# Optimization experiments

Measured on AMD Instinct MI355X. Metric: run time of the kernel, lower is better.

The kernel has to match this reference:

```python
import jax, jax.numpy as jnp
import numpy as np

N, E, T = 10000, 50000, 80000   # nodes, edges, triplets
D, H, C, CF = 16, 128, 64, 64   # n_orb, hidden_dim, conv_dim, coeffs_dim


def l2norm(v):
    # matches torch F.normalize(dim=-1): x / max(||x||_2, 1e-12)
    return v / jnp.maximum(jnp.linalg.norm(v, axis=-1, keepdims=True), 1e-12)


def setup_inputs() -> dict:
    key = jax.random.key(0)
    ks = jax.random.split(key, 16)

    def w(k, i, o):
        return jax.random.normal(k, (i, o), jnp.float32) / np.sqrt(i).astype(np.float32)

    return {
        "x": jax.random.normal(ks[0], (N, H), jnp.float32),
        "cji": jax.random.normal(ks[1], (E, D, CF), jnp.float32),
        "robs": jax.random.normal(ks[2], (E, D), jnp.float32),
        "shbs": jax.random.normal(ks[3], (T, D), jnp.float32),
        "idx_i": jax.random.randint(ks[4], (E,), 0, N),
        "idx_j": jax.random.randint(ks[5], (E,), 0, N),
        "tri_idx_k": jax.random.randint(ks[6], (T,), 0, N),
        "edge_idx_kj": jax.random.randint(ks[7], (T,), 0, E),
        "edge_idx_ji": jax.random.randint(ks[8], (T,), 0, E),
        "W_nb": w(ks[9], H, 2 * C), "b_nb": jnp.zeros((2 * C,), jnp.float32),
        "W_c1": w(ks[10], CF, C),
        "W_c2": w(ks[11], C, 2 * C),
        "W_t3": w(ks[12], C, C), "b_t3": jnp.zeros((C,), jnp.float32),
        "W_n1": w(ks[13], 2 * C, C), "b_n1": jnp.zeros((C,), jnp.float32),
        "W_n2": w(ks[14], C, C), "b_n2": jnp.zeros((C,), jnp.float32),
        "W_na": w(ks[15], C, H),
    }


def reference(x, cji, robs, shbs, idx_i, idx_j, tri_idx_k, edge_idx_kj,
              edge_idx_ji, W_nb, b_nb, W_c1, W_c2, W_t3, b_t3, W_n1, b_n1,
              W_n2, b_n2, W_na):
    silu = jax.nn.silu
    # node_before_lin + chunk
    h = x @ W_nb + b_nb                       # [N, 2C]
    xq, xk = jnp.split(h, 2, axis=-1)         # each [N, C]
    # coeffs_before_lin: act -> Dense -> act -> Dense (no biases)
    c = silu(silu(cji) @ W_c1) @ W_c2         # [E, D, 2C]
    cji2, ckj = jnp.split(c, 2, axis=-1)      # each [E, D, C]
    # triplet gathers
    ckj_g = l2norm(ckj[edge_idx_kj])          # [T, D, C]
    tbo = l2norm(jnp.einsum('td,tdh->th', shbs * robs[edge_idx_kj], ckj_g))  # [T, C]
    tbw = tbo * jax.nn.sigmoid(xk[tri_idx_k])  # [T, C]
    # scatter triplets -> edges (dim_size = robs.size(0) = E)
    agg = jax.ops.segment_sum(tbw, edge_idx_ji, num_segments=E)  # [E, C]
    tbw2 = silu(agg) @ W_t3 + b_t3            # three_lin, [E, C]
    cji3 = l2norm(cji2 * (1.0 + tbw2[:, None, :]))  # cji + cji*w, normalized
    lcao = l2norm(jnp.einsum('ed,edh->eh', robs, cji3))  # [E, C]
    # node message: node_lin on concatenated endpoint features
    m = jnp.concatenate([xq[idx_i], xq[idx_j]], axis=-1)  # [E, 2C]
    m = silu(silu(m) @ W_n1 + b_n1) @ W_n2 + b_n2          # [E, C]
    out = x + jax.ops.segment_sum(lcao * m, idx_i, num_segments=N) @ W_na
    return out
```

## Files before the change

kernel.cpp:

```cpp
#include <hip/hip_runtime.h>
#include <hip/hip_bf16.h>

#define NN 10000
#define EE 50000
#define TT 80000
#define DD 16
#define HH 128
#define CC 64

typedef __hip_bfloat16 bf16;
typedef __attribute__((ext_vector_type(8))) short bf16x8;
typedef __attribute__((ext_vector_type(4))) short bf16x4;
typedef __attribute__((ext_vector_type(4))) float f32x4;

__device__ __forceinline__ float silu_f(float x) {
  return x * __builtin_amdgcn_rcpf(1.f + __expf(-x));
}
__device__ __forceinline__ float sigm_f(float x) {
  return __builtin_amdgcn_rcpf(1.f + __expf(-x));
}

__device__ __forceinline__ short f2bs(float x) {
  __hip_bfloat16 h = __float2bfloat16(x);
  short s;
  __builtin_memcpy(&s, &h, 2);
  return s;
}

__device__ __forceinline__ float rnorm_f(float ss) {
  return __builtin_amdgcn_rcpf(fmaxf(__builtin_amdgcn_sqrtf(ss), 1e-12f));
}

__device__ __forceinline__ void bf2x(unsigned u, float& lo, float& hi) {
  lo = __uint_as_float(u << 16);
  hi = __uint_as_float(u & 0xffff0000u);
}

#define ZERO_U4 960000

#define K2_BLOCKS 2048
#define K2_TILES 50000
__global__ __launch_bounds__(256, 2) void k_coeffs(
    const float* __restrict__ cji, const float* __restrict__ W_c1,
    const float* __restrict__ W_c2, bf16* __restrict__ cji2,
    bf16* __restrict__ ckjn, const float* __restrict__ x,
    const float* __restrict__ W_nb, const float* __restrict__ b_nb,
    float* __restrict__ sxq, float* __restrict__ sigxk,
    uint4* __restrict__ zero_p) {
  __shared__ __align__(16) float xs[16][HH];
  const int tid = threadIdx.x;
  const int bid = blockIdx.x;
  const int w = tid >> 6, l = tid & 63;
  const int lr = l & 15, lg = l >> 4;

  for (int i = bid * 256 + tid; i < ZERO_U4; i += K2_BLOCKS * 256)
    zero_p[i] = (uint4){0u, 0u, 0u, 0u};

  if (bid < NN / 16) {
    const int g = tid >> 7, c = tid & 127;
    const int nb = bid * 16 + g * 8;
#pragma unroll
    for (int i = 0; i < 8; ++i)
      xs[g * 8 + i][c] = x[(size_t)(nb + i) * HH + c];
    __syncthreads();
    float acc[8];
    const float bb = b_nb[c];
#pragma unroll
    for (int i = 0; i < 8; ++i) acc[i] = bb;
    for (int k = 0; k < HH; k += 4) {
      const float w0 = W_nb[(k + 0) * HH + c];
      const float w1 = W_nb[(k + 1) * HH + c];
      const float w2 = W_nb[(k + 2) * HH + c];
      const float w3 = W_nb[(k + 3) * HH + c];
#pragma unroll
      for (int i = 0; i < 8; ++i) {
        const float4 xv = *(const float4*)(&xs[g * 8 + i][k]);
        acc[i] = fmaf(xv.x, w0, acc[i]);
        acc[i] = fmaf(xv.y, w1, acc[i]);
        acc[i] = fmaf(xv.z, w2, acc[i]);
        acc[i] = fmaf(xv.w, w3, acc[i]);
      }
    }
    if (c < CC) {
#pragma unroll
      for (int i = 0; i < 8; ++i)
        sxq[(size_t)(nb + i) * CC + c] = silu_f(acc[i]);
    } else {
#pragma unroll
      for (int i = 0; i < 8; ++i)
        sigxk[(size_t)(nb + i) * CC + (c - CC)] = sigm_f(acc[i]);
    }
  }

  bf16x4 bw1[4][4];
  bf16x4 bw2[4][8];
#pragma unroll
  for (int rt = 0; rt < 4; ++rt)
#pragma unroll
    for (int kt = 0; kt < 4; ++kt) {
      bf16x4 t;
#pragma unroll
      for (int b = 0; b < 4; ++b)
        t[b] = f2bs(W_c1[(kt * 16 + lg * 4 + b) * 64 + rt * 16 + lr]);
      bw1[rt][kt] = t;
    }
#pragma unroll
  for (int kt = 0; kt < 4; ++kt)
#pragma unroll
    for (int ct = 0; ct < 8; ++ct) {
      bf16x4 t;
#pragma unroll
      for (int b = 0; b < 4; ++b)
        t[b] = f2bs(W_c2[(kt * 16 + lg * 4 + b) * 128 + ct * 16 + lr]);
      bw2[kt][ct] = t;
    }

  const int nwave = K2_BLOCKS * 4;
  int tile = bid * 4 + w;
  if (tile >= K2_TILES) return;

  float4 r[4];
#pragma unroll
  for (int kt = 0; kt < 4; ++kt)
    r[kt] = *(const float4*)(cji + (size_t)tile * 1024 + lr * 64 + kt * 16 + lg * 4);

  for (; tile < K2_TILES; tile += nwave) {
    bf16x4 sB[4];
#pragma unroll
    for (int kt = 0; kt < 4; ++kt) {
      bf16x4 t;
      t[0] = f2bs(silu_f(r[kt].x));
      t[1] = f2bs(silu_f(r[kt].y));
      t[2] = f2bs(silu_f(r[kt].z));
      t[3] = f2bs(silu_f(r[kt].w));
      sB[kt] = t;
    }

    const int next = tile + nwave;
    if (next < K2_TILES) {
#pragma unroll
      for (int kt = 0; kt < 4; ++kt)
        r[kt] = *(const float4*)(cji + (size_t)next * 1024 + lr * 64 + kt * 16 + lg * 4);
    }

    f32x4 acc1[4];
#pragma unroll
    for (int rt = 0; rt < 4; ++rt) acc1[rt] = (f32x4){0.f, 0.f, 0.f, 0.f};
    __builtin_amdgcn_s_setprio(1);
#pragma unroll
    for (int rt = 0; rt < 4; ++rt)
#pragma unroll
      for (int kt = 0; kt < 4; ++kt)
        acc1[rt] = __builtin_amdgcn_mfma_f32_16x16x16bf16_1k(bw1[rt][kt], sB[kt], acc1[rt], 0, 0, 0);
    __builtin_amdgcn_s_setprio(0);

    bf16x4 tf[4];
#pragma unroll
    for (int kt = 0; kt < 4; ++kt) {
      bf16x4 t;
#pragma unroll
      for (int b = 0; b < 4; ++b) t[b] = f2bs(silu_f(acc1[kt][b]));
      tf[kt] = t;
    }

    f32x4 acc2[8];
#pragma unroll
    for (int ct = 0; ct < 8; ++ct) acc2[ct] = (f32x4){0.f, 0.f, 0.f, 0.f};
    __builtin_amdgcn_s_setprio(1);
#pragma unroll
    for (int ct = 0; ct < 8; ++ct)
#pragma unroll
      for (int kt = 0; kt < 4; ++kt)
        acc2[ct] = __builtin_amdgcn_mfma_f32_16x16x16bf16_1k(tf[kt], bw2[kt][ct], acc2[ct], 0, 0, 0);
    __builtin_amdgcn_s_setprio(0);

    float rn[4];
#pragma unroll
    for (int j = 0; j < 4; ++j) {
      float ss = acc2[4][j] * acc2[4][j];
      ss = fmaf(acc2[5][j], acc2[5][j], ss);
      ss = fmaf(acc2[6][j], acc2[6][j], ss);
      ss = fmaf(acc2[7][j], acc2[7][j], ss);
#pragma unroll
      for (int m = 1; m < 16; m <<= 1) ss += __shfl_xor(ss, m, 64);
      rn[j] = rnorm_f(ss);
    }

    union { short h[16]; uint4 u[2]; } p;
#pragma unroll
    for (int ct = 0; ct < 4; ++ct)
#pragma unroll
      for (int j = 0; j < 4; ++j) p.h[ct * 4 + j] = f2bs(acc2[ct][j]);
    {
      uint4* d0 = (uint4*)(cji2 + (size_t)tile * 1024 + l * 16);
      d0[0] = p.u[0];
      d0[1] = p.u[1];
    }
#pragma unroll
    for (int ct = 0; ct < 4; ++ct)
#pragma unroll
      for (int j = 0; j < 4; ++j) p.h[ct * 4 + j] = f2bs(acc2[4 + ct][j] * rn[j]);
    {
      uint4* d1 = (uint4*)(ckjn + (size_t)tile * 1024 + l * 16);
      d1[0] = p.u[0];
      d1[1] = p.u[1];
    }
  }
}

#define K3_WAVES 20000
__global__ __launch_bounds__(256) void k_triplet(
    const bf16* __restrict__ ckjn, const float* __restrict__ shbs,
    const float* __restrict__ robs, const float* __restrict__ sigxk,
    const int* __restrict__ tri_idx_k, const int* __restrict__ edge_idx_kj,
    const int* __restrict__ edge_idx_ji, float* __restrict__ agg) {
  const int wid = (blockIdx.x * 256 + threadIdx.x) >> 6;
  const int l = threadIdx.x & 63;
  if (wid >= K3_WAVES) return;
  const int lq = l >> 4;
  const int t0 = wid * 4;

  int kj[4], kn[4], ji[4];
#pragma unroll
  for (int i = 0; i < 4; ++i) {
    kj[i] = edge_idx_kj[t0 + i];
    kn[i] = tri_idx_k[t0 + i];
    ji[i] = edge_idx_ji[t0 + i];
  }
  float4 sh[4], rb[4];
  uint4 u0[4], u1[4];
  float sx[4];
#pragma unroll
  for (int i = 0; i < 4; ++i) {
    sh[i] = *(const float4*)(shbs + (size_t)(t0 + i) * DD + lq * 4);
    rb[i] = *(const float4*)(robs + (size_t)kj[i] * DD + lq * 4);
    const uint4* b = (const uint4*)(ckjn + (size_t)kj[i] * 1024 + l * 16);
    u0[i] = b[0];
    u1[i] = b[1];
    sx[i] = sigxk[(size_t)kn[i] * CC + l];
  }

  float acc[4][4];
#pragma unroll
  for (int i = 0; i < 4; ++i) {
    const float w0 = sh[i].x * rb[i].x, w1 = sh[i].y * rb[i].y,
                w2 = sh[i].z * rb[i].z, w3 = sh[i].w * rb[i].w;
    float x0, x1, x2, x3;
    bf2x(u0[i].x, x0, x1); bf2x(u0[i].y, x2, x3);
    acc[i][0] = fmaf(w3, x3, fmaf(w2, x2, fmaf(w1, x1, w0 * x0)));
    bf2x(u0[i].z, x0, x1); bf2x(u0[i].w, x2, x3);
    acc[i][1] = fmaf(w3, x3, fmaf(w2, x2, fmaf(w1, x1, w0 * x0)));
    bf2x(u1[i].x, x0, x1); bf2x(u1[i].y, x2, x3);
    acc[i][2] = fmaf(w3, x3, fmaf(w2, x2, fmaf(w1, x1, w0 * x0)));
    bf2x(u1[i].z, x0, x1); bf2x(u1[i].w, x2, x3);
    acc[i][3] = fmaf(w3, x3, fmaf(w2, x2, fmaf(w1, x1, w0 * x0)));
  }
#pragma unroll
  for (int m = 16; m < 64; m <<= 1)
#pragma unroll
    for (int i = 0; i < 4; ++i)
#pragma unroll
      for (int q = 0; q < 4; ++q) acc[i][q] += __shfl_xor(acc[i][q], m, 64);

  float sel[4], ss[4];
#pragma unroll
  for (int i = 0; i < 4; ++i) {
    sel[i] = (lq == 0) ? acc[i][0] : (lq == 1) ? acc[i][1]
             : (lq == 2) ? acc[i][2] : acc[i][3];
    ss[i] = sel[i] * sel[i];
  }
#pragma unroll
  for (int m = 1; m < 64; m <<= 1)
#pragma unroll
    for (int i = 0; i < 4; ++i) ss[i] += __shfl_xor(ss[i], m, 64);
#pragma unroll
  for (int i = 0; i < 4; ++i) {
    const float tbw = sel[i] * rnorm_f(ss[i]) * sx[i];
    atomicAdd(&agg[(size_t)ji[i] * CC + l], tbw);
  }
}

#define K4A_TILES 3125
#define K4A_BLOCKS 256
__global__ __launch_bounds__(256, 2) void k_edge_a(
    const float* __restrict__ agg, const float* __restrict__ sxq,
    const int* __restrict__ idx_i, const int* __restrict__ idx_j,
    const float* __restrict__ W_t3, const float* __restrict__ b_t3,
    const float* __restrict__ W_n1, const float* __restrict__ b_n1,
    const float* __restrict__ W_n2, const float* __restrict__ b_n2,
    float* __restrict__ onew_buf, float* __restrict__ m_buf) {
  __shared__ __align__(16) float fbuf[4][16 * 68];
  __shared__ __align__(16) short sbuf[4][16 * 72];
  const int tid = threadIdx.x;
  const int w = tid >> 6, l = tid & 63;
  const int lr = l & 15, lg = l >> 4;
  float* fb = fbuf[w];
  short* sb = sbuf[w];

  bf16x8 bt3[2][4], bn1[4][4], bn2[2][4];
#pragma unroll
  for (int kt = 0; kt < 2; ++kt)
#pragma unroll
    for (int nt = 0; nt < 4; ++nt) {
      bf16x8 t;
#pragma unroll
      for (int b = 0; b < 8; ++b)
        t[b] = f2bs(W_t3[(kt * 32 + lg * 8 + b) * 64 + nt * 16 + lr]);
      bt3[kt][nt] = t;
    }
#pragma unroll
  for (int kt = 0; kt < 4; ++kt)
#pragma unroll
    for (int nt = 0; nt < 4; ++nt) {
      bf16x8 t;
#pragma unroll
      for (int b = 0; b < 8; ++b)
        t[b] = f2bs(W_n1[(kt * 32 + lg * 8 + b) * 64 + nt * 16 + lr]);
      bn1[kt][nt] = t;
    }
#pragma unroll
  for (int kt = 0; kt < 2; ++kt)
#pragma unroll
    for (int nt = 0; nt < 4; ++nt) {
      bf16x8 t;
#pragma unroll
      for (int b = 0; b < 8; ++b)
        t[b] = f2bs(W_n2[(kt * 32 + lg * 8 + b) * 64 + nt * 16 + lr]);
      bn2[kt][nt] = t;
    }
  float bt3c[4], bn1c[4], bn2c[4];
#pragma unroll
  for (int nt = 0; nt < 4; ++nt) {
    bt3c[nt] = b_t3[nt * 16 + lr];
    bn1c[nt] = b_n1[nt * 16 + lr];
    bn2c[nt] = b_n2[nt * 16 + lr];
  }

  for (int tile = blockIdx.x * 4 + w; tile < K4A_TILES; tile += K4A_BLOCKS * 4) {
    const int e = tile * 16 + lr;
    const int vi = idx_i[e], vj = idx_j[e];

    bf16x8 aagg[2];
#pragma unroll
    for (int kt = 0; kt < 2; ++kt) {
      const float4 u = *(const float4*)(agg + (size_t)e * 64 + kt * 32 + lg * 8);
      const float4 v = *(const float4*)(agg + (size_t)e * 64 + kt * 32 + lg * 8 + 4);
      bf16x8 t;
      t[0] = f2bs(silu_f(u.x)); t[1] = f2bs(silu_f(u.y));
      t[2] = f2bs(silu_f(u.z)); t[3] = f2bs(silu_f(u.w));
      t[4] = f2bs(silu_f(v.x)); t[5] = f2bs(silu_f(v.y));
      t[6] = f2bs(silu_f(v.z)); t[7] = f2bs(silu_f(v.w));
      aagg[kt] = t;
    }
    f32x4 acc[4];
#pragma unroll
    for (int nt = 0; nt < 4; ++nt) acc[nt] = (f32x4){0.f, 0.f, 0.f, 0.f};
#pragma unroll
    for (int nt = 0; nt < 4; ++nt) {
      acc[nt] = __builtin_amdgcn_mfma_f32_16x16x32_bf16(aagg[0], bt3[0][nt], acc[nt], 0, 0, 0);
      acc[nt] = __builtin_amdgcn_mfma_f32_16x16x32_bf16(aagg[1], bt3[1][nt], acc[nt], 0, 0, 0);
    }
#pragma unroll
    for (int nt = 0; nt < 4; ++nt)
#pragma unroll
      for (int j = 0; j < 4; ++j)
        fb[(lg * 4 + j) * 68 + nt * 16 + lr] = 1.f + bt3c[nt] + acc[nt][j];
    {
      const int row = l >> 2, cs = (l & 3) * 16;
      float* dst = onew_buf + (size_t)(tile * 16 + row) * 64 + cs;
#pragma unroll
      for (int q = 0; q < 4; ++q)
        *(float4*)(dst + q * 4) = *(const float4*)(fb + row * 68 + cs + q * 4);
    }

    bf16x8 am[4];
#pragma unroll
    for (int kt = 0; kt < 4; ++kt) {
      const float* src = (kt < 2) ? (sxq + (size_t)vi * 64 + kt * 32)
                                  : (sxq + (size_t)vj * 64 + (kt - 2) * 32);
      const float4 u = *(const float4*)(src + lg * 8);
      const float4 v = *(const float4*)(src + lg * 8 + 4);
      bf16x8 t;
      t[0] = f2bs(u.x); t[1] = f2bs(u.y); t[2] = f2bs(u.z); t[3] = f2bs(u.w);
      t[4] = f2bs(v.x); t[5] = f2bs(v.y); t[6] = f2bs(v.z); t[7] = f2bs(v.w);
      am[kt] = t;
    }
    f32x4 acc1[4];
#pragma unroll
    for (int nt = 0; nt < 4; ++nt) acc1[nt] = (f32x4){0.f, 0.f, 0.f, 0.f};
#pragma unroll
    for (int nt = 0; nt < 4; ++nt)
#pragma unroll
      for (int kt = 0; kt < 4; ++kt)
        acc1[nt] = __builtin_amdgcn_mfma_f32_16x16x32_bf16(am[kt], bn1[kt][nt], acc1[nt], 0, 0, 0);

#pragma unroll
    for (int nt = 0; nt < 4; ++nt)
#pragma unroll
      for (int j = 0; j < 4; ++j)
        sb[(lg * 4 + j) * 72 + nt * 16 + lr] = f2bs(silu_f(acc1[nt][j] + bn1c[nt]));
    const bf16x8 a20 = *(const bf16x8*)(sb + lr * 72 + lg * 8);
    const bf16x8 a21 = *(const bf16x8*)(sb + lr * 72 + 32 + lg * 8);

    f32x4 acc2[4];
#pragma unroll
    for (int nt = 0; nt < 4; ++nt) acc2[nt] = (f32x4){0.f, 0.f, 0.f, 0.f};
#pragma unroll
    for (int nt = 0; nt < 4; ++nt) {
      acc2[nt] = __builtin_amdgcn_mfma_f32_16x16x32_bf16(a20, bn2[0][nt], acc2[nt], 0, 0, 0);
      acc2[nt] = __builtin_amdgcn_mfma_f32_16x16x32_bf16(a21, bn2[1][nt], acc2[nt], 0, 0, 0);
    }
#pragma unroll
    for (int nt = 0; nt < 4; ++nt)
#pragma unroll
      for (int j = 0; j < 4; ++j)
        fb[(lg * 4 + j) * 68 + nt * 16 + lr] = acc2[nt][j] + bn2c[nt];
    {
      const int row = l >> 2, cs = (l & 3) * 16;
      float* dst = m_buf + (size_t)(tile * 16 + row) * 64 + cs;
#pragma unroll
      for (int q = 0; q < 4; ++q)
        *(float4*)(dst + q * 4) = *(const float4*)(fb + row * 68 + cs + q * 4);
    }
  }
}

#define K4B_WAVES 25000
__global__ __launch_bounds__(256) void k_edge_b(
    const bf16* __restrict__ cji2, const float* __restrict__ robs,
    const float* __restrict__ onew_buf, const float* __restrict__ m_buf,
    const int* __restrict__ idx_i, float* __restrict__ lacc) {
  const int wid = (blockIdx.x * 256 + threadIdx.x) >> 6;
  const int l = threadIdx.x & 63;
  if (wid >= K4B_WAVES) return;
  const int lq = l >> 4, lr = l & 15;
  const int e0 = wid * 2;

  uint4 u0[2], u1[2];
  float4 rb[2];
  float ow[2][4], mm[2];
  int vi[2];
#pragma unroll
  for (int i = 0; i < 2; ++i) {
    const uint4* base = (const uint4*)(cji2 + (size_t)(e0 + i) * 1024 + l * 16);
    u0[i] = base[0];
    u1[i] = base[1];
    const float* ob = onew_buf + (size_t)(e0 + i) * 64 + lr;
    ow[i][0] = ob[0]; ow[i][1] = ob[16]; ow[i][2] = ob[32]; ow[i][3] = ob[48];
    rb[i] = *(const float4*)(robs + (size_t)(e0 + i) * DD + lq * 4);
    mm[i] = m_buf[(size_t)(e0 + i) * 64 + l];
    vi[i] = idx_i[e0 + i];
  }

  float v[2][16];
#pragma unroll
  for (int i = 0; i < 2; ++i) {
    bf2x(u0[i].x, v[i][0], v[i][1]);   bf2x(u0[i].y, v[i][2], v[i][3]);
    bf2x(u0[i].z, v[i][4], v[i][5]);   bf2x(u0[i].w, v[i][6], v[i][7]);
    bf2x(u1[i].x, v[i][8], v[i][9]);   bf2x(u1[i].y, v[i][10], v[i][11]);
    bf2x(u1[i].z, v[i][12], v[i][13]); bf2x(u1[i].w, v[i][14], v[i][15]);
#pragma unroll
    for (int j = 0; j < 4; ++j) {
      v[i][j] *= ow[i][0];
      v[i][4 + j] *= ow[i][1];
      v[i][8 + j] *= ow[i][2];
      v[i][12 + j] *= ow[i][3];
    }
  }
  float sq[2][4];
#pragma unroll
  for (int i = 0; i < 2; ++i)
#pragma unroll
    for (int j = 0; j < 4; ++j)
      sq[i][j] = fmaf(v[i][j], v[i][j],
                 fmaf(v[i][4 + j], v[i][4 + j],
                 fmaf(v[i][8 + j], v[i][8 + j], v[i][12 + j] * v[i][12 + j])));
#pragma unroll
  for (int m = 1; m < 16; m <<= 1)
#pragma unroll
    for (int i = 0; i < 2; ++i)
#pragma unroll
      for (int j = 0; j < 4; ++j) sq[i][j] += __shfl_xor(sq[i][j], m, 64);

  float lcq[2][4];
#pragma unroll
  for (int i = 0; i < 2; ++i) {
    const float t0 = rb[i].x * rnorm_f(sq[i][0]),
                t1 = rb[i].y * rnorm_f(sq[i][1]),
                t2 = rb[i].z * rnorm_f(sq[i][2]),
                t3 = rb[i].w * rnorm_f(sq[i][3]);
#pragma unroll
    for (int q = 0; q < 4; ++q)
      lcq[i][q] = fmaf(t0, v[i][q * 4 + 0],
                  fmaf(t1, v[i][q * 4 + 1],
                  fmaf(t2, v[i][q * 4 + 2], t3 * v[i][q * 4 + 3])));
  }
#pragma unroll
  for (int m = 16; m < 64; m <<= 1)
#pragma unroll
    for (int i = 0; i < 2; ++i)
#pragma unroll
      for (int q = 0; q < 4; ++q) lcq[i][q] += __shfl_xor(lcq[i][q], m, 64);

  float sel[2], ss[2];
#pragma unroll
  for (int i = 0; i < 2; ++i) {
    sel[i] = (lq == 0) ? lcq[i][0] : (lq == 1) ? lcq[i][1]
             : (lq == 2) ? lcq[i][2] : lcq[i][3];
    ss[i] = sel[i] * sel[i];
  }
#pragma unroll
  for (int m = 1; m < 64; m <<= 1)
#pragma unroll
    for (int i = 0; i < 2; ++i) ss[i] += __shfl_xor(ss[i], m, 64);
#pragma unroll
  for (int i = 0; i < 2; ++i) {
    const float lcao = sel[i] * rnorm_f(ss[i]);
    atomicAdd(&lacc[(size_t)vi[i] * CC + l], lcao * mm[i]);
  }
}

__global__ __launch_bounds__(128) void k_out(
    const float* __restrict__ x, const float* __restrict__ lacc,
    const float* __restrict__ W_na, float* __restrict__ out) {
  __shared__ __align__(16) float ls[8][CC];
  const int t = threadIdx.x;
  const int base = blockIdx.x * 8;
  for (int idx = t; idx < 8 * CC; idx += 128)
    ls[idx >> 6][idx & 63] = lacc[(size_t)(base + (idx >> 6)) * CC + (idx & 63)];
  __syncthreads();
  float acc[8];
#pragma unroll
  for (int i = 0; i < 8; ++i) acc[i] = x[(size_t)(base + i) * HH + t];
  for (int k = 0; k < CC; k += 4) {
    const float w0 = W_na[(k + 0) * HH + t];
    const float w1 = W_na[(k + 1) * HH + t];
    const float w2 = W_na[(k + 2) * HH + t];
    const float w3 = W_na[(k + 3) * HH + t];
#pragma unroll
    for (int i = 0; i < 8; ++i) {
      const float4 lv = *(const float4*)(&ls[i][k]);
      acc[i] = fmaf(lv.x, w0, acc[i]);
      acc[i] = fmaf(lv.y, w1, acc[i]);
      acc[i] = fmaf(lv.z, w2, acc[i]);
      acc[i] = fmaf(lv.w, w3, acc[i]);
    }
  }
#pragma unroll
  for (int i = 0; i < 8; ++i) out[(size_t)(base + i) * HH + t] = acc[i];
}

extern "C" void kernel_launch(void* const* d_in, const int* in_sizes, int n_in,
                              void* d_out, int out_size, void* d_ws,
                              size_t ws_size, hipStream_t stream) {
  const float* x = (const float*)d_in[0];
  const float* cji = (const float*)d_in[1];
  const float* robs = (const float*)d_in[2];
  const float* shbs = (const float*)d_in[3];
  const int* idx_i = (const int*)d_in[4];
  const int* idx_j = (const int*)d_in[5];
  const int* tri_idx_k = (const int*)d_in[6];
  const int* edge_idx_kj = (const int*)d_in[7];
  const int* edge_idx_ji = (const int*)d_in[8];
  const float* W_nb = (const float*)d_in[9];
  const float* b_nb = (const float*)d_in[10];
  const float* W_c1 = (const float*)d_in[11];
  const float* W_c2 = (const float*)d_in[12];
  const float* W_t3 = (const float*)d_in[13];
  const float* b_t3 = (const float*)d_in[14];
  const float* W_n1 = (const float*)d_in[15];
  const float* b_n1 = (const float*)d_in[16];
  const float* W_n2 = (const float*)d_in[17];
  const float* b_n2 = (const float*)d_in[18];
  const float* W_na = (const float*)d_in[19];
  float* out = (float*)d_out;

  char* ws = (char*)d_ws;
  const size_t NC4 = (size_t)NN * CC * 4;
  const size_t EDC2 = (size_t)EE * DD * CC * 2;
  const size_t EC4 = (size_t)EE * CC * 4;
  float* sxq = (float*)(ws);
  float* sigxk = (float*)(ws + NC4);
  bf16* cji2 = (bf16*)(ws + 2 * NC4);
  bf16* ckjn = (bf16*)(ws + 2 * NC4 + EDC2);
  float* agg = (float*)(ws + 2 * NC4 + 2 * EDC2);
  float* lacc = (float*)(ws + 2 * NC4 + 2 * EDC2 + EC4);
  float* onew_buf = (float*)(ws + 2 * NC4 + EDC2);
  float* m_buf = (float*)(ws + 2 * NC4 + EDC2 + EC4);

  k_coeffs<<<K2_BLOCKS, 256, 0, stream>>>(cji, W_c1, W_c2, cji2, ckjn, x,
                                          W_nb, b_nb, sxq, sigxk,
                                          (uint4*)agg);
  k_triplet<<<(K3_WAVES + 3) / 4, 256, 0, stream>>>(ckjn, shbs, robs, sigxk,
                                                    tri_idx_k, edge_idx_kj,
                                                    edge_idx_ji, agg);
  k_edge_a<<<K4A_BLOCKS, 256, 0, stream>>>(
      agg, sxq, idx_i, idx_j, W_t3, b_t3, W_n1, b_n1, W_n2, b_n2, onew_buf,
      m_buf);
  k_edge_b<<<(K4B_WAVES + 3) / 4, 256, 0, stream>>>(cji2, robs, onew_buf,
                                                    m_buf, idx_i, lacc);
  k_out<<<NN / 8, 128, 0, stream>>>(x, lacc, W_na, out);
}
```

Before: 194.1 us.

## Fuse edge MLP and LCAO scatter kernels, drop setprio in coeffs kernel

Merges k_edge_a and k_edge_b into a single k_edge kernel. The per-edge three_lin outputs and node-MLP message stay in per-wave LDS buffers instead of making a global round-trip through onew_buf/m_buf, and the LCAO normalization plus atomic scatter run inside the same tile loop. It also removes the s_setprio bracketing around the MFMA blocks in k_coeffs. The fused kernel runs on only 256 blocks with a serial 8-iteration inner loop per tile, so there is less parallelism for hiding the cji2 gather latency than the separate 25000-wave kernel had.

```diff
diff --git a/kernel.cpp b/kernel.cpp
--- a/kernel.cpp
+++ b/kernel.cpp
@@ -146,13 +146,11 @@
     f32x4 acc1[4];
 #pragma unroll
     for (int rt = 0; rt < 4; ++rt) acc1[rt] = (f32x4){0.f, 0.f, 0.f, 0.f};
-    __builtin_amdgcn_s_setprio(1);
 #pragma unroll
     for (int rt = 0; rt < 4; ++rt)
 #pragma unroll
       for (int kt = 0; kt < 4; ++kt)
         acc1[rt] = __builtin_amdgcn_mfma_f32_16x16x16bf16_1k(bw1[rt][kt], sB[kt], acc1[rt], 0, 0, 0);
-    __builtin_amdgcn_s_setprio(0);
 
     bf16x4 tf[4];
 #pragma unroll
@@ -166,13 +164,11 @@
     f32x4 acc2[8];
 #pragma unroll
     for (int ct = 0; ct < 8; ++ct) acc2[ct] = (f32x4){0.f, 0.f, 0.f, 0.f};
-    __builtin_amdgcn_s_setprio(1);
 #pragma unroll
     for (int ct = 0; ct < 8; ++ct)
 #pragma unroll
       for (int kt = 0; kt < 4; ++kt)
         acc2[ct] = __builtin_amdgcn_mfma_f32_16x16x16bf16_1k(tf[kt], bw2[kt][ct], acc2[ct], 0, 0, 0);
-    __builtin_amdgcn_s_setprio(0);
 
     float rn[4];
 #pragma unroll
@@ -280,21 +276,25 @@
   }
 }
 
-#define K4A_TILES 3125
-#define K4A_BLOCKS 256
-__global__ __launch_bounds__(256, 2) void k_edge_a(
+#define K4_TILES 3125
+#define K4_BLOCKS 256
+__global__ __launch_bounds__(256, 2) void k_edge(
     const float* __restrict__ agg, const float* __restrict__ sxq,
     const int* __restrict__ idx_i, const int* __restrict__ idx_j,
     const float* __restrict__ W_t3, const float* __restrict__ b_t3,
     const float* __restrict__ W_n1, const float* __restrict__ b_n1,
     const float* __restrict__ W_n2, const float* __restrict__ b_n2,
-    float* __restrict__ onew_buf, float* __restrict__ m_buf) {
-  __shared__ __align__(16) float fbuf[4][16 * 68];
+    const bf16* __restrict__ cji2, const float* __restrict__ robs,
+    float* __restrict__ lacc) {
+  __shared__ __align__(16) float obuf[4][16 * 68];
+  __shared__ __align__(16) float mbuf[4][16 * 68];
   __shared__ __align__(16) short sbuf[4][16 * 72];
   const int tid = threadIdx.x;
   const int w = tid >> 6, l = tid & 63;
   const int lr = l & 15, lg = l >> 4;
-  float* fb = fbuf[w];
+  const int lq = l >> 4;
+  float* ob = obuf[w];
+  float* mb = mbuf[w];
   short* sb = sbuf[w];
 
   bf16x8 bt3[2][4], bn1[4][4], bn2[2][4];
@@ -336,7 +336,7 @@
     bn2c[nt] = b_n2[nt * 16 + lr];
   }
 
-  for (int tile = blockIdx.x * 4 + w; tile < K4A_TILES; tile += K4A_BLOCKS * 4) {
+  for (int tile = blockIdx.x * 4 + w; tile < K4_TILES; tile += K4_BLOCKS * 4) {
     const int e = tile * 16 + lr;
     const int vi = idx_i[e], vj = idx_j[e];
 
@@ -364,14 +364,7 @@
     for (int nt = 0; nt < 4; ++nt)
 #pragma unroll
       for (int j = 0; j < 4; ++j)
-        fb[(lg * 4 + j) * 68 + nt * 16 + lr] = 1.f + bt3c[nt] + acc[nt][j];
-    {
-      const int row = l >> 2, cs = (l & 3) * 16;
-      float* dst = onew_buf + (size_t)(tile * 16 + row) * 64 + cs;
-#pragma unroll
-      for (int q = 0; q < 4; ++q)
-        *(float4*)(dst + q * 4) = *(const float4*)(fb + row * 68 + cs + q * 4);
-    }
+        ob[(lg * 4 + j) * 68 + nt * 16 + lr] = 1.f + bt3c[nt] + acc[nt][j];
 
     bf16x8 am[4];
 #pragma unroll
@@ -414,109 +407,100 @@
     for (int nt = 0; nt < 4; ++nt)
 #pragma unroll
       for (int j = 0; j < 4; ++j)
-        fb[(lg * 4 + j) * 68 + nt * 16 + lr] = acc2[nt][j] + bn2c[nt];
-    {
-      const int row = l >> 2, cs = (l & 3) * 16;
-      float* dst = m_buf + (size_t)(tile * 16 + row) * 64 + cs;
-#pragma unroll
-      for (int q = 0; q < 4; ++q)
-        *(float4*)(dst + q * 4) = *(const float4*)(fb + row * 68 + cs + q * 4);
-    }
-  }
-}
-
-#define K4B_WAVES 25000
-__global__ __launch_bounds__(256) void k_edge_b(
-    const bf16* __restrict__ cji2, const float* __restrict__ robs,
-    const float* __restrict__ onew_buf, const float* __restrict__ m_buf,
-    const int* __restrict__ idx_i, float* __restrict__ lacc) {
-  const int wid = (blockIdx.x * 256 + threadIdx.x) >> 6;
-  const int l = threadIdx.x & 63;
-  if (wid >= K4B_WAVES) return;
-  const int lq = l >> 4, lr = l & 15;
-  const int e0 = wid * 2;
-
-  uint4 u0[2], u1[2];
-  float4 rb[2];
-  float ow[2][4], mm[2];
-  int vi[2];
-#pragma unroll
-  for (int i = 0; i < 2; ++i) {
-    const uint4* base = (const uint4*)(cji2 + (size_t)(e0 + i) * 1024 + l * 16);
-    u0[i] = base[0];
-    u1[i] = base[1];
-    const float* ob = onew_buf + (size_t)(e0 + i) * 64 + lr;
-    ow[i][0] = ob[0]; ow[i][1] = ob[16]; ow[i][2] = ob[32]; ow[i][3] = ob[48];
-    rb[i] = *(const float4*)(robs + (size_t)(e0 + i) * DD + lq * 4);
-    mm[i] = m_buf[(size_t)(e0 + i) * 64 + l];
-    vi[i] = idx_i[e0 + i];
-  }
-
-  float v[2][16];
-#pragma unroll
-  for (int i = 0; i < 2; ++i) {
-    bf2x(u0[i].x, v[i][0], v[i][1]);   bf2x(u0[i].y, v[i][2], v[i][3]);
-    bf2x(u0[i].z, v[i][4], v[i][5]);   bf2x(u0[i].w, v[i][6], v[i][7]);
-    bf2x(u1[i].x, v[i][8], v[i][9]);   bf2x(u1[i].y, v[i][10], v[i][11]);
-    bf2x(u1[i].z, v[i][12], v[i][13]); bf2x(u1[i].w, v[i][14], v[i][15]);
-#pragma unroll
-    for (int j = 0; j < 4; ++j) {
-      v[i][j] *= ow[i][0];
-      v[i][4 + j] *= ow[i][1];
-      v[i][8 + j] *= ow[i][2];
-      v[i][12 + j] *= ow[i][3];
-    }
-  }
-  float sq[2][4];
-#pragma unroll
-  for (int i = 0; i < 2; ++i)
-#pragma unroll
-    for (int j = 0; j < 4; ++j)
-      sq[i][j] = fmaf(v[i][j], v[i][j],
-                 fmaf(v[i][4 + j], v[i][4 + j],
-                 fmaf(v[i][8 + j], v[i][8 + j], v[i][12 + j] * v[i][12 + j])));
-#pragma unroll
-  for (int m = 1; m < 16; m <<= 1)
-#pragma unroll
-    for (int i = 0; i < 2; ++i)
-#pragma unroll
-      for (int j = 0; j < 4; ++j) sq[i][j] += __shfl_xor(sq[i][j], m, 64);
-
-  float lcq[2][4];
-#pragma unroll
-  for (int i = 0; i < 2; ++i) {
-    const float t0 = rb[i].x * rnorm_f(sq[i][0]),
-                t1 = rb[i].y * rnorm_f(sq[i][1]),
-                t2 = rb[i].z * rnorm_f(sq[i][2]),
-                t3 = rb[i].w * rnorm_f(sq[i][3]);
-#pragma unroll
-    for (int q = 0; q < 4; ++q)
-      lcq[i][q] = fmaf(t0, v[i][q * 4 + 0],
-                  fmaf(t1, v[i][q * 4 + 1],
-                  fmaf(t2, v[i][q * 4 + 2], t3 * v[i][q * 4 + 3])));
-  }
-#pragma unroll
-  for (int m = 16; m < 64; m <<= 1)
-#pragma unroll
-    for (int i = 0; i < 2; ++i)
-#pragma unroll
-      for (int q = 0; q < 4; ++q) lcq[i][q] += __shfl_xor(lcq[i][q], m, 64);
-
-  float sel[2], ss[2];
-#pragma unroll
-  for (int i = 0; i < 2; ++i) {
-    sel[i] = (lq == 0) ? lcq[i][0] : (lq == 1) ? lcq[i][1]
-             : (lq == 2) ? lcq[i][2] : lcq[i][3];
-    ss[i] = sel[i] * sel[i];
-  }
-#pragma unroll
-  for (int m = 1; m < 64; m <<= 1)
-#pragma unroll
-    for (int i = 0; i < 2; ++i) ss[i] += __shfl_xor(ss[i], m, 64);
-#pragma unroll
-  for (int i = 0; i < 2; ++i) {
-    const float lcao = sel[i] * rnorm_f(ss[i]);
-    atomicAdd(&lacc[(size_t)vi[i] * CC + l], lcao * mm[i]);
+        mb[(lg * 4 + j) * 68 + nt * 16 + lr] = acc2[nt][j] + bn2c[nt];
+
+#pragma unroll 1
+    for (int pp = 0; pp < 8; ++pp) {
+      const int e0 = tile * 16 + pp * 2;
+      uint4 u0[2], u1[2];
+      float4 rb[2];
+      float ow[2][4], mm[2];
+      int vib[2];
+#pragma unroll
+      for (int i = 0; i < 2; ++i) {
+        const uint4* base =
+            (const uint4*)(cji2 + (size_t)(e0 + i) * 1024 + l * 16);
+        u0[i] = base[0];
+        u1[i] = base[1];
+        const int le = pp * 2 + i;
+        ow[i][0] = ob[le * 68 + lr];
+        ow[i][1] = ob[le * 68 + 16 + lr];
+        ow[i][2] = ob[le * 68 + 32 + lr];
+        ow[i][3] = ob[le * 68 + 48 + lr];
+        mm[i] = mb[le * 68 + l];
+        rb[i] = *(const float4*)(robs + (size_t)(e0 + i) * DD + lq * 4);
+        vib[i] = idx_i[e0 + i];
+      }
+
+      float v[2][16];
+#pragma unroll
+      for (int i = 0; i < 2; ++i) {
+        bf2x(u0[i].x, v[i][0], v[i][1]);   bf2x(u0[i].y, v[i][2], v[i][3]);
+        bf2x(u0[i].z, v[i][4], v[i][5]);   bf2x(u0[i].w, v[i][6], v[i][7]);
+        bf2x(u1[i].x, v[i][8], v[i][9]);   bf2x(u1[i].y, v[i][10], v[i][11]);
+        bf2x(u1[i].z, v[i][12], v[i][13]); bf2x(u1[i].w, v[i][14], v[i][15]);
+#pragma unroll
+        for (int j = 0; j < 4; ++j) {
+          v[i][j] *= ow[i][0];
+          v[i][4 + j] *= ow[i][1];
+          v[i][8 + j] *= ow[i][2];
+          v[i][12 + j] *= ow[i][3];
+        }
+      }
+      float sq[2][4];
+#pragma unroll
+      for (int i = 0; i < 2; ++i)
+#pragma unroll
+        for (int j = 0; j < 4; ++j)
+          sq[i][j] = fmaf(v[i][j], v[i][j],
+                     fmaf(v[i][4 + j], v[i][4 + j],
+                     fmaf(v[i][8 + j], v[i][8 + j],
+                          v[i][12 + j] * v[i][12 + j])));
+#pragma unroll
+      for (int m = 1; m < 16; m <<= 1)
+#pragma unroll
+        for (int i = 0; i < 2; ++i)
+#pragma unroll
+          for (int j = 0; j < 4; ++j) sq[i][j] += __shfl_xor(sq[i][j], m, 64);
+
+      float lcq[2][4];
+#pragma unroll
+      for (int i = 0; i < 2; ++i) {
+        const float t0 = rb[i].x * rnorm_f(sq[i][0]),
+                    t1 = rb[i].y * rnorm_f(sq[i][1]),
+                    t2 = rb[i].z * rnorm_f(sq[i][2]),
+                    t3 = rb[i].w * rnorm_f(sq[i][3]);
+#pragma unroll
+        for (int q = 0; q < 4; ++q)
+          lcq[i][q] = fmaf(t0, v[i][q * 4 + 0],
+                      fmaf(t1, v[i][q * 4 + 1],
+                      fmaf(t2, v[i][q * 4 + 2], t3 * v[i][q * 4 + 3])));
+      }
+#pragma unroll
+      for (int m = 16; m < 64; m <<= 1)
+#pragma unroll
+        for (int i = 0; i < 2; ++i)
+#pragma unroll
+          for (int q = 0; q < 4; ++q)
+            lcq[i][q] += __shfl_xor(lcq[i][q], m, 64);
+
+      float sel[2], ss[2];
+#pragma unroll
+      for (int i = 0; i < 2; ++i) {
+        sel[i] = (lq == 0) ? lcq[i][0] : (lq == 1) ? lcq[i][1]
+                 : (lq == 2) ? lcq[i][2] : lcq[i][3];
+        ss[i] = sel[i] * sel[i];
+      }
+#pragma unroll
+      for (int m = 1; m < 64; m <<= 1)
+#pragma unroll
+        for (int i = 0; i < 2; ++i) ss[i] += __shfl_xor(ss[i], m, 64);
+#pragma unroll
+      for (int i = 0; i < 2; ++i) {
+        const float lcao = sel[i] * rnorm_f(ss[i]);
+        atomicAdd(&lacc[(size_t)vib[i] * CC + l], lcao * mm[i]);
+      }
+    }
   }
 }
 
@@ -585,8 +569,6 @@
   bf16* ckjn = (bf16*)(ws + 2 * NC4 + EDC2);
   float* agg = (float*)(ws + 2 * NC4 + 2 * EDC2);
   float* lacc = (float*)(ws + 2 * NC4 + 2 * EDC2 + EC4);
-  float* onew_buf = (float*)(ws + 2 * NC4 + EDC2);
-  float* m_buf = (float*)(ws + 2 * NC4 + EDC2 + EC4);
 
   k_coeffs<<<K2_BLOCKS, 256, 0, stream>>>(cji, W_c1, W_c2, cji2, ckjn, x,
                                           W_nb, b_nb, sxq, sigxk,
@@ -594,10 +576,8 @@
   k_triplet<<<(K3_WAVES + 3) / 4, 256, 0, stream>>>(ckjn, shbs, robs, sigxk,
                                                     tri_idx_k, edge_idx_kj,
                                                     edge_idx_ji, agg);
-  k_edge_a<<<K4A_BLOCKS, 256, 0, stream>>>(
-      agg, sxq, idx_i, idx_j, W_t3, b_t3, W_n1, b_n1, W_n2, b_n2, onew_buf,
-      m_buf);
-  k_edge_b<<<(K4B_WAVES + 3) / 4, 256, 0, stream>>>(cji2, robs, onew_buf,
-                                                    m_buf, idx_i, lacc);
+  k_edge<<<K4_BLOCKS, 256, 0, stream>>>(agg, sxq, idx_i, idx_j, W_t3, b_t3,
+                                        W_n1, b_n1, W_n2, b_n2, cji2, robs,
+                                        lacc);
   k_out<<<NN / 8, 128, 0, stream>>>(x, lacc, W_na, out);
 }
```

After: 223.2 us. 1.15x slower.
